# Optimization experiments

Hardware: AMD Instinct MI355X
Metric: run time of the kernel (lower is better)

The kernel has to match this reference:

```python
import jax, jax.numpy as jnp
import numpy as np

UNITS = 512
EMB = 256

def setup_inputs() -> dict:
    key = jax.random.key(0)
    ks = jax.random.split(key, 12)
    b, t = 64, 2048
    inputs = jax.random.normal(ks[0], (b, EMB), jnp.float32)
    h_tm1 = jax.random.normal(ks[1], (b, UNITS), jnp.float32)
    context = jax.random.normal(ks[2], (b, t, UNITS), jnp.float32)
    s = 0.02
    params = {
        "Wi": jax.random.normal(ks[3], (EMB, UNITS), jnp.float32) * s,
        "bi": jnp.zeros((UNITS,), jnp.float32),
        "kernel": jax.random.normal(ks[4], (UNITS, 3 * UNITS), jnp.float32) * s,
        "recurrent_kernel": jax.random.normal(ks[5], (UNITS, 3 * UNITS), jnp.float32) * s,
        "attention_kernel": jax.random.normal(ks[6], (UNITS, 3 * UNITS), jnp.float32) * s,
        "bias": jnp.zeros((3 * UNITS,), jnp.float32),
        "Wa": jax.random.normal(ks[7], (UNITS, UNITS), jnp.float32) * s,
        "ba_w": jnp.zeros((UNITS,), jnp.float32),
        "Ua": jax.random.normal(ks[8], (UNITS, UNITS), jnp.float32) * s,
        "ba_u": jnp.zeros((UNITS,), jnp.float32),
        "Va": jax.random.normal(ks[9], (UNITS, 1), jnp.float32) * s,
        "ba_v": jnp.zeros((1,), jnp.float32),
        "Wo": jax.random.normal(ks[10], (UNITS, UNITS), jnp.float32) * s,
        "bo": jnp.zeros((UNITS,), jnp.float32),
    }
    return {"inputs": inputs, "h_tm1": h_tm1, "context": context, **params}


def reference(inputs, h_tm1, context, Wi, bi, kernel, recurrent_kernel,
              attention_kernel, bias, Wa, ba_w, Ua, ba_u, Va, ba_v, Wo, bo):
    U = UNITS
    # input dense: embedding_size != units
    x = inputs @ Wi + bi                              # [b, U]
    # gate input projections (fused then split)
    xg = x @ kernel + bias                            # [b, 3U]
    x_z, x_r, x_h = xg[:, :U], xg[:, U:2*U], xg[:, 2*U:]
    # Bahdanau attention over context using h_tm1 as query
    score = jnp.tanh(context @ Wa + ba_w + (h_tm1 @ Ua + ba_u)[:, None, :])  # [b,t,U]
    score = score @ Va + ba_v                         # [b, t, 1]
    attn = jax.nn.softmax(score, axis=1)              # [b, t, 1]
    ctx_vec = jnp.sum(attn * context, axis=1)         # [b, U]
    cg = ctx_vec @ attention_kernel                   # [b, 3U]
    c_z, c_r, c_h = cg[:, :U], cg[:, U:2*U], cg[:, 2*U:]
    rec_z = h_tm1 @ recurrent_kernel[:, :U]
    rec_r = h_tm1 @ recurrent_kernel[:, U:2*U]
    z = jax.nn.sigmoid(x_z + rec_z + c_z)
    r = jax.nn.sigmoid(x_r + rec_r + c_r)
    rec_h = (r * h_tm1) @ recurrent_kernel[:, 2*U:]
    h_bar = jnp.tanh(x_h + rec_h + c_h)
    h = z * h_tm1 + (1.0 - z) * h_bar
    out = h @ Wo + bo
    return out, h
```

## Files before the change

### kernel.cpp

```cpp
#include <hip/hip_runtime.h>

#define UNITS 512
#define EMBD  256
#define BATCH 64
#define TLEN  2048

typedef __bf16 bf16x8 __attribute__((ext_vector_type(8)));
typedef float  f32x4  __attribute__((ext_vector_type(4)));

__device__ __forceinline__ unsigned short f2bf(float x) {
  return __builtin_bit_cast(unsigned short, (__bf16)x);
}
__device__ __forceinline__ float fast_tanh(float x) {
  float e = __expf(2.0f * x);
  return __fdividef(e - 1.0f, e + 1.0f);
}
__device__ __forceinline__ float fast_sigmoid(float x) {
  return __fdividef(1.0f, 1.0f + __expf(-x));
}

__global__ void prep_kernel(const float* __restrict__ Wa,
                            unsigned short* __restrict__ WaF,
                            float* __restrict__ gO, float* __restrict__ gL) {
  int idx = blockIdx.x * 256 + threadIdx.x;
  int j  = idx & 7;
  int l  = (idx >> 3) & 63;
  int nt = (idx >> 9) & 31;
  int ks = idx >> 14;
  int k = ks * 32 + ((l >> 4) << 3) + j;
  int n = (nt << 4) + (l & 15);
  WaF[idx] = f2bf(Wa[k * 512 + n]);
  if (idx < BATCH * UNITS) gO[idx] = 0.0f;
  if (idx < BATCH)         gL[idx] = 0.0f;
}

__global__ void rowdot_kernel(const float* __restrict__ A, int lda,
                              const float* __restrict__ Bm, int ldb,
                              const float* __restrict__ b1,
                              const float* __restrict__ b2,
                              const float* __restrict__ denom,
                              float* __restrict__ out, int ldo, int K) {
  __shared__ float Asm[512];
  __shared__ float red[4][64];
  const int m  = blockIdx.y;
  const int cl = threadIdx.x & 63;
  const int ks = threadIdx.x >> 6;
  const int c  = (blockIdx.x << 6) + cl;
  float sc = 1.0f;
  if (denom) sc = __fdividef(1.0f, denom[m]);
  for (int k = threadIdx.x; k < K; k += 256) Asm[k] = A[m * lda + k] * sc;
  __syncthreads();
  const int kl = K >> 2;
  const float* bp = Bm + (size_t)(ks * kl) * ldb + c;
  float acc = 0.0f;
#pragma unroll 8
  for (int kk = 0; kk < kl; ++kk)
    acc = fmaf(Asm[ks * kl + kk], bp[(size_t)kk * ldb], acc);
  red[ks][cl] = acc;
  __syncthreads();
  if (threadIdx.x < 64) {
    int cc = (blockIdx.x << 6) + threadIdx.x;
    float v = red[0][threadIdx.x] + red[1][threadIdx.x] +
              red[2][threadIdx.x] + red[3][threadIdx.x];
    if (b1) v += b1[cc];
    if (b2) v += b2[cc];
    out[m * ldo + cc] = v;
  }
}

__launch_bounds__(256, 2)
__global__ void score_ctx_kernel(const float* __restrict__ ctx,
                                 const unsigned short* __restrict__ WaF,
                                 const float* __restrict__ uvec,
                                 const float* __restrict__ Va,
                                 float* __restrict__ gO,
                                 float* __restrict__ gL) {
  __shared__ unsigned short As[2][64][40];
  __shared__ float sS[64];
  __shared__ float sE[64];

  const int b   = blockIdx.y;
  const int tc  = blockIdx.x;
  const int tid = threadIdx.x;
  const int lane  = tid & 63;
  const int w     = tid >> 6;
  const int row_a = lane & 15;
  const int kq    = lane >> 4;

  const float* ctile = ctx + ((size_t)b * TLEN + (size_t)tc * 64) * UNITS;

  if (tid < 64) sS[tid] = 0.0f;

  f32x4 acc[4][8];
#pragma unroll
  for (int mt = 0; mt < 4; ++mt)
#pragma unroll
    for (int nt = 0; nt < 8; ++nt)
      acc[mt][nt] = (f32x4){0.0f, 0.0f, 0.0f, 0.0f};

  const int r_st = tid & 63;
  const int half = tid >> 6;

  const float4* abase = (const float4*)(ctile + r_st * UNITS + half * 8);
  const bf16x8* bbase = (const bf16x8*)WaF + lane;

  float4 pa0[2], pa1[2];
  pa0[0] = abase[0]; pa0[1] = abase[1];
  pa1[0] = abase[8]; pa1[1] = abase[9];

  bf16x8 bcur[8], bnxt[8];
#pragma unroll
  for (int nt = 0; nt < 8; ++nt)
    bcur[nt] = bbase[(size_t)((w << 3) + nt) * 64];

  {
    ushort4 q0 = make_ushort4(f2bf(pa0[0].x), f2bf(pa0[0].y), f2bf(pa0[0].z), f2bf(pa0[0].w));
    ushort4 q1 = make_ushort4(f2bf(pa0[1].x), f2bf(pa0[1].y), f2bf(pa0[1].z), f2bf(pa0[1].w));
    *(ushort4*)&As[0][r_st][half * 8]     = q0;
    *(ushort4*)&As[0][r_st][half * 8 + 4] = q1;
  }

#pragma unroll
  for (int ks = 0; ks < 16; ++ks) {
    const int cur = ks & 1;
    __syncthreads();
    bf16x8 af[4];
#pragma unroll
    for (int mt = 0; mt < 4; ++mt)
      af[mt] = *(const bf16x8*)&As[cur][mt * 16 + row_a][kq * 8];
    if (ks < 14) {
      float4* pdst = (cur == 0) ? pa0 : pa1;
      pdst[0] = abase[(ks + 2) * 8];
      pdst[1] = abase[(ks + 2) * 8 + 1];
    }
    if (ks < 15) {
#pragma unroll
      for (int nt = 0; nt < 8; ++nt)
        bnxt[nt] = bbase[(size_t)((ks + 1) * 32 + (w << 3) + nt) * 64];
    }
#pragma unroll
    for (int nt = 0; nt < 8; ++nt)
#pragma unroll
      for (int mt = 0; mt < 4; ++mt)
        acc[mt][nt] = __builtin_amdgcn_mfma_f32_16x16x32_bf16(af[mt], bcur[nt], acc[mt][nt], 0, 0, 0);
    if (ks < 15) {
      const float4* psrc = (cur == 0) ? pa1 : pa0;
      ushort4 q0 = make_ushort4(f2bf(psrc[0].x), f2bf(psrc[0].y), f2bf(psrc[0].z), f2bf(psrc[0].w));
      ushort4 q1 = make_ushort4(f2bf(psrc[1].x), f2bf(psrc[1].y), f2bf(psrc[1].z), f2bf(psrc[1].w));
      *(ushort4*)&As[1 - cur][r_st][half * 8]     = q0;
      *(ushort4*)&As[1 - cur][r_st][half * 8 + 4] = q1;
#pragma unroll
      for (int nt = 0; nt < 8; ++nt) bcur[nt] = bnxt[nt];
    }
  }

  float uvals[8], vvals[8];
#pragma unroll
  for (int nt = 0; nt < 8; ++nt) {
    int n_g = (w << 7) + (nt << 4) + row_a;
    uvals[nt] = uvec[b * UNITS + n_g];
    vvals[nt] = Va[n_g];
  }
#pragma unroll
  for (int mt = 0; mt < 4; ++mt) {
#pragma unroll
    for (int r = 0; r < 4; ++r) {
      float v = 0.0f;
#pragma unroll
      for (int nt = 0; nt < 8; ++nt)
        v += fast_tanh(acc[mt][nt][r] + uvals[nt]) * vvals[nt];
      v += __shfl_xor(v, 1);
      v += __shfl_xor(v, 2);
      v += __shfl_xor(v, 4);
      v += __shfl_xor(v, 8);
      if (row_a == 0) atomicAdd(&sS[mt * 16 + kq * 4 + r], v);
    }
  }
  __syncthreads();
  if (tid < 64) sE[tid] = __expf(sS[tid]);
  __syncthreads();
  if (tid < 64) {
    float e = sE[tid];
#pragma unroll
    for (int off = 1; off < 64; off <<= 1) e += __shfl_xor(e, off);
    if (tid == 0) atomicAdd(&gL[b], e);
  }
#pragma unroll
  for (int cc = 0; cc < 2; ++cc) {
    int c = cc * 256 + tid;
    float o = 0.0f;
#pragma unroll 8
    for (int t = 0; t < 64; ++t)
      o = fmaf(sE[t], ctile[t * UNITS + c], o);
    atomicAdd(&gO[b * UNITS + c], o);
  }
}

__global__ void gates_kernel(const float* __restrict__ xg,
                             const float* __restrict__ rec_zr,
                             const float* __restrict__ cg,
                             const float* __restrict__ h,
                             float* __restrict__ zbuf,
                             float* __restrict__ rhbuf) {
  int idx = blockIdx.x * 256 + threadIdx.x;
  int m = idx >> 9, j = idx & 511;
  float xz = xg[m * 1536 + j],        xr = xg[m * 1536 + 512 + j];
  float rz = rec_zr[m * 1024 + j],    rr = rec_zr[m * 1024 + 512 + j];
  float cz = cg[m * 1536 + j],        cr = cg[m * 1536 + 512 + j];
  float z = fast_sigmoid(xz + rz + cz);
  float r = fast_sigmoid(xr + rr + cr);
  zbuf[idx]  = z;
  rhbuf[idx] = r * h[idx];
}

__global__ void newh_kernel(const float* __restrict__ xg,
                            const float* __restrict__ rech,
                            const float* __restrict__ cg,
                            const float* __restrict__ zbuf,
                            const float* __restrict__ h,
                            float* __restrict__ hout) {
  int idx = blockIdx.x * 256 + threadIdx.x;
  int m = idx >> 9, j = idx & 511;
  float hb = fast_tanh(xg[m * 1536 + 1024 + j] + rech[idx] + cg[m * 1536 + 1024 + j]);
  float z  = zbuf[idx];
  hout[idx] = z * h[idx] + (1.0f - z) * hb;
}

extern "C" void kernel_launch(void* const* d_in, const int* in_sizes, int n_in,
                              void* d_out, int out_size, void* d_ws, size_t ws_size,
                              hipStream_t stream) {
  (void)in_sizes; (void)n_in; (void)out_size; (void)ws_size;
  const float* inputs = (const float*)d_in[0];
  const float* h_tm1  = (const float*)d_in[1];
  const float* ctx    = (const float*)d_in[2];
  const float* Wi     = (const float*)d_in[3];
  const float* bi     = (const float*)d_in[4];
  const float* kern   = (const float*)d_in[5];
  const float* rk     = (const float*)d_in[6];
  const float* ak     = (const float*)d_in[7];
  const float* bias   = (const float*)d_in[8];
  const float* Wa     = (const float*)d_in[9];
  const float* ba_w   = (const float*)d_in[10];
  const float* Ua     = (const float*)d_in[11];
  const float* ba_u   = (const float*)d_in[12];
  const float* Va     = (const float*)d_in[13];
  const float* Wo     = (const float*)d_in[15];
  const float* bo     = (const float*)d_in[16];

  float* out = (float*)d_out;
  float* ws  = (float*)d_ws;
  unsigned short* WaF = (unsigned short*)ws;
  float* gO     = ws + 131072;
  float* gL     = ws + 163840;
  float* xbuf   = ws + 163904;
  float* xg     = ws + 196672;
  float* ubuf   = ws + 294976;
  float* rec_zr = ws + 327744;
  float* cg     = ws + 393280;
  float* zbuf   = ws + 491584;
  float* rhbuf  = ws + 524352;
  float* rech   = ws + 557120;

  prep_kernel<<<1024, 256, 0, stream>>>(Wa, WaF, gO, gL);
  rowdot_kernel<<<dim3(8, 64), 256, 0, stream>>>(inputs, EMBD, Wi, UNITS, bi, nullptr, nullptr, xbuf, UNITS, EMBD);
  rowdot_kernel<<<dim3(24, 64), 256, 0, stream>>>(xbuf, UNITS, kern, 1536, bias, nullptr, nullptr, xg, 1536, UNITS);
  rowdot_kernel<<<dim3(8, 64), 256, 0, stream>>>(h_tm1, UNITS, Ua, UNITS, ba_u, ba_w, nullptr, ubuf, UNITS, UNITS);
  rowdot_kernel<<<dim3(16, 64), 256, 0, stream>>>(h_tm1, UNITS, rk, 1536, nullptr, nullptr, nullptr, rec_zr, 1024, UNITS);
  score_ctx_kernel<<<dim3(32, 64), 256, 0, stream>>>(ctx, WaF, ubuf, Va, gO, gL);
  rowdot_kernel<<<dim3(24, 64), 256, 0, stream>>>(gO, UNITS, ak, 1536, nullptr, nullptr, gL, cg, 1536, UNITS);
  gates_kernel<<<128, 256, 0, stream>>>(xg, rec_zr, cg, h_tm1, zbuf, rhbuf);
  rowdot_kernel<<<dim3(8, 64), 256, 0, stream>>>(rhbuf, UNITS, rk + 1024, 1536, nullptr, nullptr, nullptr, rech, UNITS, UNITS);
  newh_kernel<<<128, 256, 0, stream>>>(xg, rech, cg, zbuf, h_tm1, out + BATCH * UNITS);
  rowdot_kernel<<<dim3(8, 64), 256, 0, stream>>>(out + BATCH * UNITS, UNITS, Wo, UNITS, bo, nullptr, nullptr, out, UNITS, UNITS);
}
```

Before: 566.3 us.

## Merge independent prologue kernels and fuse gate elementwise into matvec kernels

Combines the Wa bf16 repack, zeroing, and three independent input/hidden matvecs into one heterogeneous launch dispatched by block index. Folds the r-gate sigmoid into the rec_h matvec's staging and the z/h_bar/h computation into the output projection's staging, which removes two elementwise kernels and their intermediate buffers. This cuts the launch count from 11 to 6 and drops some global round trips. In exchange, the gate math is recomputed redundantly in every column block.

New measurement: 543.0 us. 4.1% less time.

```diff
diff --git a/kernel.cpp b/kernel.cpp
--- a/kernel.cpp
+++ b/kernel.cpp
@@ -19,37 +19,15 @@
   return __fdividef(1.0f, 1.0f + __expf(-x));
 }
 
-__global__ void prep_kernel(const float* __restrict__ Wa,
-                            unsigned short* __restrict__ WaF,
-                            float* __restrict__ gO, float* __restrict__ gL) {
-  int idx = blockIdx.x * 256 + threadIdx.x;
-  int j  = idx & 7;
-  int l  = (idx >> 3) & 63;
-  int nt = (idx >> 9) & 31;
-  int ks = idx >> 14;
-  int k = ks * 32 + ((l >> 4) << 3) + j;
-  int n = (nt << 4) + (l & 15);
-  WaF[idx] = f2bf(Wa[k * 512 + n]);
-  if (idx < BATCH * UNITS) gO[idx] = 0.0f;
-  if (idx < BATCH)         gL[idx] = 0.0f;
-}
-
-__global__ void rowdot_kernel(const float* __restrict__ A, int lda,
-                              const float* __restrict__ Bm, int ldb,
-                              const float* __restrict__ b1,
-                              const float* __restrict__ b2,
-                              const float* __restrict__ denom,
-                              float* __restrict__ out, int ldo, int K) {
-  __shared__ float Asm[512];
-  __shared__ float red[4][64];
-  const int m  = blockIdx.y;
+__device__ __forceinline__ void dot_core(const float* Asm, float (*red)[64],
+                                         const float* __restrict__ Bm, int ldb,
+                                         const float* __restrict__ b1,
+                                         const float* __restrict__ b2,
+                                         float* __restrict__ out, int ldo,
+                                         int K, int bx, int m) {
   const int cl = threadIdx.x & 63;
   const int ks = threadIdx.x >> 6;
-  const int c  = (blockIdx.x << 6) + cl;
-  float sc = 1.0f;
-  if (denom) sc = __fdividef(1.0f, denom[m]);
-  for (int k = threadIdx.x; k < K; k += 256) Asm[k] = A[m * lda + k] * sc;
-  __syncthreads();
+  const int c  = (bx << 6) + cl;
   const int kl = K >> 2;
   const float* bp = Bm + (size_t)(ks * kl) * ldb + c;
   float acc = 0.0f;
@@ -59,13 +37,80 @@
   red[ks][cl] = acc;
   __syncthreads();
   if (threadIdx.x < 64) {
-    int cc = (blockIdx.x << 6) + threadIdx.x;
+    int cc = (bx << 6) + threadIdx.x;
     float v = red[0][threadIdx.x] + red[1][threadIdx.x] +
               red[2][threadIdx.x] + red[3][threadIdx.x];
     if (b1) v += b1[cc];
     if (b2) v += b2[cc];
-    out[m * ldo + cc] = v;
-  }
+    out[(size_t)m * ldo + cc] = v;
+  }
+}
+
+__global__ void stage1_kernel(const float* __restrict__ Wa,
+                              unsigned short* __restrict__ WaF,
+                              float* __restrict__ gO, float* __restrict__ gL,
+                              const float* __restrict__ inputs,
+                              const float* __restrict__ Wi,
+                              const float* __restrict__ bi,
+                              float* __restrict__ xbuf,
+                              const float* __restrict__ h_tm1,
+                              const float* __restrict__ Ua,
+                              const float* __restrict__ ba_u,
+                              const float* __restrict__ ba_w,
+                              float* __restrict__ ubuf,
+                              const float* __restrict__ rk,
+                              float* __restrict__ rec_zr) {
+  __shared__ float Asm[512];
+  __shared__ float red[4][64];
+  int bid = blockIdx.x;
+  if (bid < 1024) {
+    int idx = bid * 256 + threadIdx.x;
+    int j  = idx & 7;
+    int l  = (idx >> 3) & 63;
+    int nt = (idx >> 9) & 31;
+    int ks = idx >> 14;
+    int k = ks * 32 + ((l >> 4) << 3) + j;
+    int n = (nt << 4) + (l & 15);
+    WaF[idx] = f2bf(Wa[k * 512 + n]);
+    if (idx < BATCH * UNITS) gO[idx] = 0.0f;
+    if (idx < BATCH)         gL[idx] = 0.0f;
+    return;
+  }
+  bid -= 1024;
+  if (bid < 512) {
+    int bx = bid & 7, m = bid >> 3;
+    for (int k = threadIdx.x; k < 256; k += 256) Asm[k] = inputs[m * 256 + k];
+    __syncthreads();
+    dot_core(Asm, red, Wi, 512, bi, nullptr, xbuf, 512, 256, bx, m);
+    return;
+  }
+  bid -= 512;
+  if (bid < 512) {
+    int bx = bid & 7, m = bid >> 3;
+    for (int k = threadIdx.x; k < 512; k += 256) Asm[k] = h_tm1[m * 512 + k];
+    __syncthreads();
+    dot_core(Asm, red, Ua, 512, ba_u, ba_w, ubuf, 512, 512, bx, m);
+    return;
+  }
+  bid -= 512;
+  {
+    int bx = bid & 15, m = bid >> 4;
+    for (int k = threadIdx.x; k < 512; k += 256) Asm[k] = h_tm1[m * 512 + k];
+    __syncthreads();
+    dot_core(Asm, red, rk, 1536, nullptr, nullptr, rec_zr, 1024, 512, bx, m);
+  }
+}
+
+__global__ void xg_kernel(const float* __restrict__ xbuf,
+                          const float* __restrict__ kern,
+                          const float* __restrict__ bias,
+                          float* __restrict__ xg) {
+  __shared__ float Asm[512];
+  __shared__ float red[4][64];
+  int m = blockIdx.y;
+  for (int k = threadIdx.x; k < 512; k += 256) Asm[k] = xbuf[m * 512 + k];
+  __syncthreads();
+  dot_core(Asm, red, kern, 1536, bias, nullptr, xg, 1536, 512, blockIdx.x, m);
 }
 
 __launch_bounds__(256, 2)
@@ -196,34 +241,59 @@
   }
 }
 
-__global__ void gates_kernel(const float* __restrict__ xg,
-                             const float* __restrict__ rec_zr,
-                             const float* __restrict__ cg,
-                             const float* __restrict__ h,
-                             float* __restrict__ zbuf,
-                             float* __restrict__ rhbuf) {
-  int idx = blockIdx.x * 256 + threadIdx.x;
-  int m = idx >> 9, j = idx & 511;
-  float xz = xg[m * 1536 + j],        xr = xg[m * 1536 + 512 + j];
-  float rz = rec_zr[m * 1024 + j],    rr = rec_zr[m * 1024 + 512 + j];
-  float cz = cg[m * 1536 + j],        cr = cg[m * 1536 + 512 + j];
-  float z = fast_sigmoid(xz + rz + cz);
-  float r = fast_sigmoid(xr + rr + cr);
-  zbuf[idx]  = z;
-  rhbuf[idx] = r * h[idx];
-}
-
-__global__ void newh_kernel(const float* __restrict__ xg,
-                            const float* __restrict__ rech,
+__global__ void cg_kernel(const float* __restrict__ gO,
+                          const float* __restrict__ gL,
+                          const float* __restrict__ ak,
+                          float* __restrict__ cg) {
+  __shared__ float Asm[512];
+  __shared__ float red[4][64];
+  int m = blockIdx.y;
+  float sc = __fdividef(1.0f, gL[m]);
+  for (int k = threadIdx.x; k < 512; k += 256) Asm[k] = gO[m * 512 + k] * sc;
+  __syncthreads();
+  dot_core(Asm, red, ak, 1536, nullptr, nullptr, cg, 1536, 512, blockIdx.x, m);
+}
+
+__global__ void rech_kernel(const float* __restrict__ xg,
+                            const float* __restrict__ reczr,
                             const float* __restrict__ cg,
-                            const float* __restrict__ zbuf,
                             const float* __restrict__ h,
-                            float* __restrict__ hout) {
-  int idx = blockIdx.x * 256 + threadIdx.x;
-  int m = idx >> 9, j = idx & 511;
-  float hb = fast_tanh(xg[m * 1536 + 1024 + j] + rech[idx] + cg[m * 1536 + 1024 + j]);
-  float z  = zbuf[idx];
-  hout[idx] = z * h[idx] + (1.0f - z) * hb;
+                            const float* __restrict__ rkh,
+                            float* __restrict__ out) {
+  __shared__ float Asm[512];
+  __shared__ float red[4][64];
+  int m = blockIdx.y;
+  for (int k = threadIdx.x; k < 512; k += 256) {
+    float r = fast_sigmoid(xg[m * 1536 + 512 + k] + reczr[m * 1024 + 512 + k] +
+                           cg[m * 1536 + 512 + k]);
+    Asm[k] = r * h[m * 512 + k];
+  }
+  __syncthreads();
+  dot_core(Asm, red, rkh, 1536, nullptr, nullptr, out, 512, 512, blockIdx.x, m);
+}
+
+__global__ void out_kernel(const float* __restrict__ xg,
+                           const float* __restrict__ reczr,
+                           const float* __restrict__ cg,
+                           const float* __restrict__ rech,
+                           const float* __restrict__ h_tm1,
+                           const float* __restrict__ Wo,
+                           const float* __restrict__ bo,
+                           float* __restrict__ out,
+                           float* __restrict__ hout) {
+  __shared__ float Asm[512];
+  __shared__ float red[4][64];
+  int m = blockIdx.y;
+  for (int k = threadIdx.x; k < 512; k += 256) {
+    float z  = fast_sigmoid(xg[m * 1536 + k] + reczr[m * 1024 + k] + cg[m * 1536 + k]);
+    float hb = fast_tanh(xg[m * 1536 + 1024 + k] + rech[m * 512 + k] +
+                         cg[m * 1536 + 1024 + k]);
+    float hn = z * h_tm1[m * 512 + k] + (1.0f - z) * hb;
+    Asm[k] = hn;
+    if (blockIdx.x == 0) hout[m * 512 + k] = hn;
+  }
+  __syncthreads();
+  dot_core(Asm, red, Wo, 512, bo, nullptr, out, 512, 512, blockIdx.x, m);
 }
 
 extern "C" void kernel_launch(void* const* d_in, const int* in_sizes, int n_in,
@@ -257,19 +327,16 @@
   float* ubuf   = ws + 294976;
   float* rec_zr = ws + 327744;
   float* cg     = ws + 393280;
-  float* zbuf   = ws + 491584;
-  float* rhbuf  = ws + 524352;
-  float* rech   = ws + 557120;
-
-  prep_kernel<<<1024, 256, 0, stream>>>(Wa, WaF, gO, gL);
-  rowdot_kernel<<<dim3(8, 64), 256, 0, stream>>>(inputs, EMBD, Wi, UNITS, bi, nullptr, nullptr, xbuf, UNITS, EMBD);
-  rowdot_kernel<<<dim3(24, 64), 256, 0, stream>>>(xbuf, UNITS, kern, 1536, bias, nullptr, nullptr, xg, 1536, UNITS);
-  rowdot_kernel<<<dim3(8, 64), 256, 0, stream>>>(h_tm1, UNITS, Ua, UNITS, ba_u, ba_w, nullptr, ubuf, UNITS, UNITS);
-  rowdot_kernel<<<dim3(16, 64), 256, 0, stream>>>(h_tm1, UNITS, rk, 1536, nullptr, nullptr, nullptr, rec_zr, 1024, UNITS);
+  float* rech   = ws + 491584;
+
+  stage1_kernel<<<3072, 256, 0, stream>>>(Wa, WaF, gO, gL,
+                                          inputs, Wi, bi, xbuf,
+                                          h_tm1, Ua, ba_u, ba_w, ubuf,
+                                          rk, rec_zr);
+  xg_kernel<<<dim3(24, 64), 256, 0, stream>>>(xbuf, kern, bias, xg);
   score_ctx_kernel<<<dim3(32, 64), 256, 0, stream>>>(ctx, WaF, ubuf, Va, gO, gL);
-  rowdot_kernel<<<dim3(24, 64), 256, 0, stream>>>(gO, UNITS, ak, 1536, nullptr, nullptr, gL, cg, 1536, UNITS);
-  gates_kernel<<<128, 256, 0, stream>>>(xg, rec_zr, cg, h_tm1, zbuf, rhbuf);
-  rowdot_kernel<<<dim3(8, 64), 256, 0, stream>>>(rhbuf, UNITS, rk + 1024, 1536, nullptr, nullptr, nullptr, rech, UNITS, UNITS);
-  newh_kernel<<<128, 256, 0, stream>>>(xg, rech, cg, zbuf, h_tm1, out + BATCH * UNITS);
-  rowdot_kernel<<<dim3(8, 64), 256, 0, stream>>>(out + BATCH * UNITS, UNITS, Wo, UNITS, bo, nullptr, nullptr, out, UNITS, UNITS);
-}
+  cg_kernel<<<dim3(24, 64), 256, 0, stream>>>(gO, gL, ak, cg);
+  rech_kernel<<<dim3(8, 64), 256, 0, stream>>>(xg, rec_zr, cg, h_tm1, rk + 1024, rech);
+  out_kernel<<<dim3(8, 64), 256, 0, stream>>>(xg, rec_zr, cg, rech, h_tm1, Wo, bo,
+                                              out, out + BATCH * UNITS);
+}
```
